# Optimization experiments

Hardware: AMD Instinct MI355X
Metric: run time of the kernel (lower is better)

The kernel has to match this reference:

```python
import jax, jax.numpy as jnp
import numpy as np

EPS = 1e-5
NEG_SLOPE = 0.2  # DGL GATConv default leaky_relu slope


def conv1d_same(x, w, b):
    # x: [N, Cin, T], w: [Cout, Cin, K]
    y = jax.lax.conv_general_dilated(x, w, (1,), 'SAME',
                                     dimension_numbers=('NCW', 'OIW', 'NCW'))
    return y + b[None, :, None]


def gated_conv(x, w1, b1, w2, b2, w3, b3):
    # Temporal_Gated_Conv: relu(conv1(x)*sigmoid(conv2(x)) + conv3(x))
    return jax.nn.relu(conv1d_same(x, w1, b1) * jax.nn.sigmoid(conv1d_same(x, w2, b2))
                       + conv1d_same(x, w3, b3))


def bn3(x, g, b):
    # BatchNorm1d on [N, C, T]: stats over (N, T), training mode (batch stats)
    m = jnp.mean(x, (0, 2), keepdims=True)
    v = jnp.var(x, (0, 2), keepdims=True)
    return (x - m) * jax.lax.rsqrt(v + EPS) * g[None, :, None] + b[None, :, None]


def bn2(x, g, b):
    # BatchNorm1d on [N, F]: stats over N
    m = jnp.mean(x, 0, keepdims=True)
    v = jnp.var(x, 0, keepdims=True)
    return (x - m) * jax.lax.rsqrt(v + EPS) * g[None, :] + b[None, :]


def setup_inputs() -> dict:
    key = jax.random.key(0)
    ks = jax.random.split(key, 24)
    N, C, T, H, DEG = 20000, 32, 8, 4, 16
    F = C * T          # GAT in/out feats per head = 256
    E = N * DEG
    s = 0.05
    inp = {
        'X': jax.random.normal(ks[0], (N, C, T), jnp.float32),
        'src': jax.random.randint(ks[1], (E,), 0, N, jnp.int32),
        'dst': jax.random.randint(ks[2], (E,), 0, N, jnp.int32),
        # residual_proj: Conv1d(C->C, k=1)
        'rp_w': jax.random.normal(ks[3], (C, C, 1), jnp.float32) * s,
        'rp_b': jnp.zeros((C,), jnp.float32),
        # gated_conv1: three Conv1d(C->C, k=3)
        'g1_w1': jax.random.normal(ks[4], (C, C, 3), jnp.float32) * s,
        'g1_b1': jnp.zeros((C,), jnp.float32),
        'g1_w2': jax.random.normal(ks[5], (C, C, 3), jnp.float32) * s,
        'g1_b2': jnp.zeros((C,), jnp.float32),
        'g1_w3': jax.random.normal(ks[6], (C, C, 3), jnp.float32) * s,
        'g1_b3': jnp.zeros((C,), jnp.float32),
        'bn0_g': jnp.ones((C,), jnp.float32),
        'bn0_b': jnp.zeros((C,), jnp.float32),
        # GATConv: fc [H*F, F], attn_l/attn_r [H, F], bias [H*F]
        'gat_w': jax.random.normal(ks[7], (H * F, F), jnp.float32) * s,
        'attn_l': jax.random.normal(ks[8], (H, F), jnp.float32) * s,
        'attn_r': jax.random.normal(ks[9], (H, F), jnp.float32) * s,
        'gat_bias': jnp.zeros((H * F,), jnp.float32),
        'bn1_g': jnp.ones((H * F,), jnp.float32),
        'bn1_b': jnp.zeros((H * F,), jnp.float32),
        # gated_conv2: three Conv1d(C*H -> C, k=3)
        'g2_w1': jax.random.normal(ks[10], (C, C * H, 3), jnp.float32) * s,
        'g2_b1': jnp.zeros((C,), jnp.float32),
        'g2_w2': jax.random.normal(ks[11], (C, C * H, 3), jnp.float32) * s,
        'g2_b2': jnp.zeros((C,), jnp.float32),
        'g2_w3': jax.random.normal(ks[12], (C, C * H, 3), jnp.float32) * s,
        'g2_b3': jnp.zeros((C,), jnp.float32),
        'bn2_g': jnp.ones((C,), jnp.float32),
        'bn2_b': jnp.zeros((C,), jnp.float32),
    }
    return inp


def reference(X, src, dst, rp_w, rp_b, g1_w1, g1_b1, g1_w2, g1_b2, g1_w3, g1_b3,
              bn0_g, bn0_b, gat_w, attn_l, attn_r, gat_bias, bn1_g, bn1_b,
              g2_w1, g2_b1, g2_w2, g2_b2, g2_w3, g2_b3, bn2_g, bn2_b):
    N, C, T = X.shape
    H, F = attn_l.shape

    residual = conv1d_same(X, rp_w, rp_b)                      # [N, C, T]
    x = gated_conv(X, g1_w1, g1_b1, g1_w2, g1_b2, g1_w3, g1_b3)
    x = bn3(x, bn0_g, bn0_b)
    x = x.reshape(N, C * T)                                    # row-major flatten == torch .view

    # --- DGL GATConv (feat_drop=attn_drop=0, concat heads, ReLU activation) ---
    h = (x @ gat_w.T).reshape(N, H, F)                         # fc projection
    el = jnp.sum(h * attn_l, -1)                               # [N, H]
    er = jnp.sum(h * attn_r, -1)                               # [N, H]
    e = jax.nn.leaky_relu(el[src] + er[dst], NEG_SLOPE)        # [E, H]
    # segment softmax over incoming edges of each dst node
    m = jax.ops.segment_max(e, dst, num_segments=N)            # [N, H]
    ee = jnp.exp(e - m[dst])
    den = jax.ops.segment_sum(ee, dst, num_segments=N)         # [N, H]
    alpha = ee / den[dst]                                      # [E, H]
    rst = jax.ops.segment_sum(alpha[:, :, None] * h[src], dst, num_segments=N)  # [N, H, F]
    rst = jax.nn.relu(rst + gat_bias.reshape(H, F))

    x = rst.reshape(N, H * F)                                  # concat heads
    x = bn2(x, bn1_g, bn1_b)
    x = x.reshape(N, (H * F) // T, T)                          # [N, C*H, T]
    x = gated_conv(x, g2_w1, g2_b1, g2_w2, g2_b2, g2_w3, g2_b3)
    x = bn3(x, bn2_g, bn2_b)
    x = jax.nn.relu(x + residual)                              # self.last=True, dropout=0
    return x
```

## Files before the change

### kernel.cpp

```cpp
#include <hip/hip_runtime.h>
#include <stdint.h>

#define NN 20000
#define NE 320000

typedef unsigned short us16;
typedef __attribute__((ext_vector_type(8))) short short8;
typedef __attribute__((ext_vector_type(4))) float f32x4;

union U4 { uint4 v; us16 s[8]; unsigned u[4]; };
union U2 { uint2 v; us16 s[4]; };

__device__ __forceinline__ float b2f(us16 u){ return __uint_as_float(((unsigned)u)<<16); }
__device__ __forceinline__ us16 f2b(float f){
  unsigned u = __float_as_uint(f);
  u += 0x7fffu + ((u>>16)&1u);
  return (us16)(u>>16);
}

__global__ __launch_bounds__(256) void k_misc(
    const float* __restrict__ gatw, us16* __restrict__ Wb,
    const float* __restrict__ w1, const float* __restrict__ w2, const float* __restrict__ w3,
    us16* __restrict__ Wt,
    const float* __restrict__ c1w1, const float* __restrict__ c1w2, const float* __restrict__ c1w3,
    const float* __restrict__ rp_w, us16* __restrict__ Wt1,
    const float* __restrict__ attnl, const float* __restrict__ attnr,
    float* __restrict__ wl, float* __restrict__ wr,
    const int* __restrict__ dst, int* __restrict__ counts)
{
  const int b = blockIdx.x, tid = threadIdx.x;
  if(b < 256){
    int i = b*256 + tid;
    float4 v = *(const float4*)(gatw + (size_t)i*4);
    U2 o;
    o.s[0]=f2b(v.x); o.s[1]=f2b(v.y); o.s[2]=f2b(v.z); o.s[3]=f2b(v.w);
    *(uint2*)(Wb + (size_t)i*4) = o.v;
  } else if(b < 400){
    int i = (b-256)*256 + tid;
    int s = i/12288, rem = i%12288;
    int co3 = rem>>7, ci = rem&127;
    const float* w = (co3<32) ? w1 : (co3<64) ? w2 : w3;
    Wt[i] = f2b(w[(co3&31)*384 + ci*3 + s]);
  } else if(b < 448){
    int i = (b-400)*256 + tid;
    int s = i>>12, rem = i&4095;
    int co3 = rem>>5, ci = rem&31;
    float v;
    if(co3 < 96){
      const float* w = (co3<32) ? c1w1 : (co3<64) ? c1w2 : c1w3;
      v = w[(co3&31)*96 + ci*3 + s];
    } else {
      v = (s==1) ? rp_w[(co3-96)*32 + ci] : 0.f;
    }
    Wt1[i] = f2b(v);
  } else if(b < 480){
    int bb = b-448;
    int sel = bb>>4, hd = (bb>>2)&3, fq = bb&3;
    const float* attn = sel ? attnr : attnl;
    int k = tid;
    float s = 0.f;
    int f0 = fq*64;
    #pragma unroll 8
    for(int f=f0; f<f0+64; f++)
      s = fmaf(attn[hd*256+f], gatw[(size_t)(hd*256+f)*256 + k], s);
    atomicAdd(&((sel ? wr : wl)[hd*256+k]), s);
  } else {
    int e = (b-480)*256 + tid;
    if(e < NE) atomicAdd(&counts[dst[e]], 1);
  }
}

__global__ __launch_bounds__(256) void k_gemm1(
    const float* __restrict__ X, const us16* __restrict__ Wt1,
    const float* __restrict__ b1, const float* __restrict__ b2, const float* __restrict__ b3,
    const float* __restrict__ rp_b,
    us16* __restrict__ gc1, us16* __restrict__ resid,
    float* __restrict__ bn0_sum, float* __restrict__ bn0_sq,
    const int* __restrict__ counts, int* __restrict__ offsets, int* __restrict__ cursor)
{
  __shared__ float smemF[5760];
  __shared__ float redS[32], redQ[32];
  __shared__ int wred[4];
  const int tid = threadIdx.x;
  if(blockIdx.x < 1250){
    us16* As = (us16*)smemF;
    us16* Bs = As + 6400;
    if(tid<32){ redS[tid]=0.f; redQ[tid]=0.f; }
    const int node0 = blockIdx.x*16;
    const int lane = tid&63, wv = tid>>6;
    const int mrow = lane&15, kg = (lane>>4)*8;
    for(int idx=tid; idx<1024; idx+=256){
      int n = idx>>6, rem = idx&63, slot = (rem>>5)*9, ci = rem&31;
      As[n*400 + slot*40 + ci] = 0;
    }
    #pragma unroll
    for(int i=0;i<4;i++){
      int idx = i*256 + tid;
      int n = idx>>6, rem = idx&63, ci = rem>>1, tq = rem&1;
      float4 xv = *(const float4*)(X + (size_t)(node0+n)*256 + ci*8 + tq*4);
      us16* p = &As[n*400 + (tq*4+1)*40 + ci];
      p[0]   = f2b(xv.x);
      p[40]  = f2b(xv.y);
      p[80]  = f2b(xv.z);
      p[120] = f2b(xv.w);
    }
    f32x4 acc[2][8] = {};
    for(int s=0; s<3; s++){
      if(s) __syncthreads();
      #pragma unroll
      for(int i=0;i<2;i++){
        int c = i*256 + tid;
        int co = c>>2, cq = c&3;
        *(uint4*)&Bs[co*40 + cq*8] = *(const uint4*)(Wt1 + s*4096 + co*32 + cq*8);
      }
      __syncthreads();
      short8 af[2], bfr[8];
      #pragma unroll
      for(int i=0;i<2;i++){
        int r = wv*32 + i*16 + mrow;
        af[i] = *(const short8*)&As[(r>>3)*400 + ((r&7)+s)*40 + kg];
      }
      #pragma unroll
      for(int j=0;j<8;j++)
        bfr[j] = *(const short8*)&Bs[(j*16 + mrow)*40 + kg];
      #pragma unroll
      for(int i=0;i<2;i++){
        #pragma unroll
        for(int j=0;j<8;j++)
          acc[i][j] = __builtin_amdgcn_mfma_f32_16x16x32_bf16(af[i], bfr[j], acc[i][j], 0, 0, 0);
      }
    }
    __syncthreads();
    us16* Og = (us16*)smemF;
    us16* Or = Og + 4096;
    const int coA = lane&15, coB = coA+16;
    const float b1A=b1[coA], b2A=b2[coA], b3A=b3[coA], brA=rp_b[coA];
    const float b1B=b1[coB], b2B=b2[coB], b3B=b3[coB], brB=rp_b[coB];
    float sA=0.f, qA=0.f, sB=0.f, qB=0.f;
    const int g = lane>>4;
    #pragma unroll
    for(int i=0;i<2;i++){
      int node = wv*4 + i*2 + (g>>1);
      int t0 = (g&1)*4;
      U2 pA, pB, rA2, rB2;
      #pragma unroll
      for(int r=0;r<4;r++){
        float c1 = acc[i][0][r]+b1A, c2 = acc[i][2][r]+b2A, c3 = acc[i][4][r]+b3A;
        float rr = acc[i][6][r]+brA;
        float sg = 1.f/(1.f+__expf(-c2));
        float v = fmaf(c1,sg,c3); v = v>0.f ? v : 0.f;
        sA += v; qA += v*v;
        pA.s[r]=f2b(v); rA2.s[r]=f2b(rr);
        c1 = acc[i][1][r]+b1B; c2 = acc[i][3][r]+b2B; c3 = acc[i][5][r]+b3B;
        rr = acc[i][7][r]+brB;
        sg = 1.f/(1.f+__expf(-c2));
        v = fmaf(c1,sg,c3); v = v>0.f ? v : 0.f;
        sB += v; qB += v*v;
        pB.s[r]=f2b(v); rB2.s[r]=f2b(rr);
      }
      *(uint2*)&Og[node*256 + coA*8 + t0] = pA.v;
      *(uint2*)&Og[node*256 + coB*8 + t0] = pB.v;
      *(uint2*)&Or[node*256 + coA*8 + t0] = rA2.v;
      *(uint2*)&Or[node*256 + coB*8 + t0] = rB2.v;
    }
    sA += __shfl_xor(sA,16,64); sA += __shfl_xor(sA,32,64);
    qA += __shfl_xor(qA,16,64); qA += __shfl_xor(qA,32,64);
    sB += __shfl_xor(sB,16,64); sB += __shfl_xor(sB,32,64);
    qB += __shfl_xor(qB,16,64); qB += __shfl_xor(qB,32,64);
    if(lane < 16){
      atomicAdd(&redS[coA], sA); atomicAdd(&redQ[coA], qA);
      atomicAdd(&redS[coB], sB); atomicAdd(&redQ[coB], qB);
    }
    __syncthreads();
    #pragma unroll
    for(int i=0;i<2;i++){
      int idx = i*256 + tid;
      *(uint4*)(gc1   + (size_t)node0*256 + (size_t)idx*8) = *(const uint4*)&Og[idx*8];
      *(uint4*)(resid + (size_t)node0*256 + (size_t)idx*8) = *(const uint4*)&Or[idx*8];
    }
    if(tid<32)      atomicAdd(&bn0_sum[tid], redS[tid]);
    else if(tid<64) atomicAdd(&bn0_sq[tid-32], redQ[tid-32]);
  } else {
    const int lane = tid&63, wv = tid>>6;
    int running = 0;
    int4 cur;
    {
      int idx = tid*4;
      cur = *(const int4*)(counts + idx);
    }
    for(int t=0; t<20; t++){
      int4 nxt; nxt.x=0; nxt.y=0; nxt.z=0; nxt.w=0;
      if(t < 19){
        int idx = (t+1)*1024 + tid*4;
        if(idx+3 < NN) nxt = *(const int4*)(counts + idx);
        else {
          if(idx   < NN) nxt.x = counts[idx];
          if(idx+1 < NN) nxt.y = counts[idx+1];
          if(idx+2 < NN) nxt.z = counts[idx+2];
          if(idx+3 < NN) nxt.w = counts[idx+3];
        }
      }
      int s = cur.x + cur.y + cur.z + cur.w;
      int incl = s;
      #pragma unroll
      for(int off=1; off<64; off<<=1){
        int v = __shfl_up(incl, off, 64);
        if(lane >= off) incl += v;
      }
      if(lane==63) wred[wv] = incl;
      __syncthreads();
      int woff = 0, btot = 0;
      #pragma unroll
      for(int w2=0; w2<4; w2++){
        int x = wred[w2];
        btot += x;
        if(w2 < wv) woff += x;
      }
      int e0 = running + woff + incl - s;
      int idx = t*1024 + tid*4;
      int4 o; o.x=e0; o.y=e0+cur.x; o.z=o.y+cur.y; o.w=o.z+cur.z;
      if(idx+3 < NN){
        *(int4*)(offsets+idx) = o;
        *(int4*)(cursor+idx)  = o;
      } else {
        if(idx   < NN){ offsets[idx]  =o.x; cursor[idx]  =o.x; }
        if(idx+1 < NN){ offsets[idx+1]=o.y; cursor[idx+1]=o.y; }
        if(idx+2 < NN){ offsets[idx+2]=o.z; cursor[idx+2]=o.z; }
        if(idx+3 < NN){ offsets[idx+3]=o.w; cursor[idx+3]=o.w; }
      }
      running += btot;
      cur = nxt;
      __syncthreads();
    }
    if(tid==0) offsets[NN] = running;
  }
}

__global__ __launch_bounds__(256) void k_eler2(const us16* __restrict__ gc1,
    const float* __restrict__ bn0_sum, const float* __restrict__ bn0_sq,
    const float* __restrict__ bn0g, const float* __restrict__ bn0b,
    const float* __restrict__ wl, const float* __restrict__ wr,
    float* __restrict__ el, float* __restrict__ er)
{
  __shared__ float sa[32], sb[32];
  const int tid = threadIdx.x;
  if(tid<32){
    float m = bn0_sum[tid]*(1.f/160000.f);
    float v = bn0_sq[tid]*(1.f/160000.f) - m*m;
    float a = bn0g[tid]*rsqrtf(v + 1e-5f);
    sa[tid] = a; sb[tid] = bn0b[tid] - m*a;
  }
  __syncthreads();
  const int wv = tid>>6, lane = tid&63;
  const int node = blockIdx.x*4 + wv;
  U2 g; g.v = *(const uint2*)(gc1 + (size_t)node*256 + lane*4);
  const float a = sa[lane>>1], b = sb[lane>>1];
  float xv[4];
  #pragma unroll
  for(int j=0;j<4;j++) xv[j] = fmaf(a, b2f(g.s[j]), b);
  float res[8];
  #pragma unroll
  for(int hd=0; hd<4; hd++){
    float4 lv = *(const float4*)(wl + hd*256 + lane*4);
    float4 rv = *(const float4*)(wr + hd*256 + lane*4);
    res[hd]   = xv[0]*lv.x + xv[1]*lv.y + xv[2]*lv.z + xv[3]*lv.w;
    res[4+hd] = xv[0]*rv.x + xv[1]*rv.y + xv[2]*rv.z + xv[3]*rv.w;
  }
  #pragma unroll
  for(int o=32;o;o>>=1){
    #pragma unroll
    for(int k=0;k<8;k++) res[k] += __shfl_xor(res[k], o, 64);
  }
  if(lane==0){
    #pragma unroll
    for(int hd=0;hd<4;hd++){ el[node*4+hd]=res[hd]; er[node*4+hd]=res[4+hd]; }
  }
}

__global__ __launch_bounds__(256) void k_scatter(const int* __restrict__ src, const int* __restrict__ dst,
    int* __restrict__ cursor, int* __restrict__ esrc,
    const float* __restrict__ el, const float* __restrict__ er,
    float* __restrict__ ew)
{
  int e = blockIdx.x*256 + threadIdx.x;
  if(e < NE){
    int s = src[e], d = dst[e];
    int pos = atomicAdd(&cursor[d], 1);
    esrc[pos] = s;
    float4 lv = *(const float4*)(el + s*4);
    float4 rv = *(const float4*)(er + d*4);
    float4 sc;
    sc.x = lv.x+rv.x; sc.x = sc.x>0.f ? sc.x : 0.2f*sc.x;
    sc.y = lv.y+rv.y; sc.y = sc.y>0.f ? sc.y : 0.2f*sc.y;
    sc.z = lv.z+rv.z; sc.z = sc.z>0.f ? sc.z : 0.2f*sc.z;
    sc.w = lv.w+rv.w; sc.w = sc.w>0.f ? sc.w : 0.2f*sc.w;
    *(float4*)(ew + (size_t)pos*4) = sc;
  }
}

__global__ __launch_bounds__(256) void k_agg2(
    const int* __restrict__ offsets, const int* __restrict__ esrc,
    const float* __restrict__ ew, const us16* __restrict__ gc1,
    const float* __restrict__ bn0_sum, const float* __restrict__ bn0_sq,
    const float* __restrict__ bn0g, const float* __restrict__ bn0b,
    us16* __restrict__ Axg)
{
  const int tid = threadIdx.x;
  const int wv = tid>>6, lane = tid&63;
  const int node = blockIdx.x*4 + wv;
  const int ch = lane>>1;
  float mmn = bn0_sum[ch]*(1.f/160000.f);
  float vvn = bn0_sq[ch]*(1.f/160000.f) - mmn*mmn;
  float sa = bn0g[ch]*rsqrtf(vvn + 1e-5f);
  float sb = bn0b[ch] - mmn*sa;
  const int beg = offsets[node];
  const int deg = offsets[node+1] - beg;
  const int h = lane>>4, i0 = lane&15;
  float m = -3.0e38f;
  for(int i=i0; i<deg; i+=16) m = fmaxf(m, ew[(size_t)(beg+i)*4 + h]);
  m = fmaxf(m, __shfl_xor(m,1,64)); m = fmaxf(m, __shfl_xor(m,2,64));
  m = fmaxf(m, __shfl_xor(m,4,64)); m = fmaxf(m, __shfl_xor(m,8,64));
  float den = 0.f;
  for(int i=i0; i<deg; i+=16) den += __expf(ew[(size_t)(beg+i)*4 + h] - m);
  den += __shfl_xor(den,1,64); den += __shfl_xor(den,2,64);
  den += __shfl_xor(den,4,64); den += __shfl_xor(den,8,64);
  const float m0=__shfl(m,0,64),   m1=__shfl(m,16,64),  m2=__shfl(m,32,64),  m3=__shfl(m,48,64);
  const float d0=__shfl(den,0,64), d1=__shfl(den,16,64),d2=__shfl(den,32,64),d3=__shfl(den,48,64);
  const float v0=d0>0.f?1.f/d0:0.f, v1=d1>0.f?1.f/d1:0.f,
              v2=d2>0.f?1.f/d2:0.f, v3=d3>0.f?1.f/d3:0.f;
  float a0c[4]={},a1c[4]={},a2c[4]={},a3c[4]={};
  #pragma unroll 4
  for(int j=0; j<deg; j++){
    int pos = beg+j;
    float4 w4 = *(const float4*)(ew + (size_t)pos*4);
    int sN = esrc[pos];
    U2 hv; hv.v = *(const uint2*)(gc1 + (size_t)sN*256 + lane*4);
    float e0 = __expf(w4.x-m0)*v0;
    float e1 = __expf(w4.y-m1)*v1;
    float e2 = __expf(w4.z-m2)*v2;
    float e3 = __expf(w4.w-m3)*v3;
    #pragma unroll
    for(int kk=0;kk<4;kk++){
      float x = b2f(hv.s[kk]);
      a0c[kk] = fmaf(e0,x,a0c[kk]);
      a1c[kk] = fmaf(e1,x,a1c[kk]);
      a2c[kk] = fmaf(e2,x,a2c[kk]);
      a3c[kk] = fmaf(e3,x,a3c[kk]);
    }
  }
  const float sbi = sb * ((deg>0)?1.f:0.f);
  U2 o0,o1,o2,o3;
  #pragma unroll
  for(int kk=0;kk<4;kk++){
    o0.s[kk]=f2b(fmaf(sa,a0c[kk],sbi));
    o1.s[kk]=f2b(fmaf(sa,a1c[kk],sbi));
    o2.s[kk]=f2b(fmaf(sa,a2c[kk],sbi));
    o3.s[kk]=f2b(fmaf(sa,a3c[kk],sbi));
  }
  *(uint2*)(Axg + ((size_t)node)*256            + lane*4) = o0.v;
  *(uint2*)(Axg + ((size_t)NN + node)*256       + lane*4) = o1.v;
  *(uint2*)(Axg + ((size_t)2*NN + node)*256     + lane*4) = o2.v;
  *(uint2*)(Axg + ((size_t)3*NN + node)*256     + lane*4) = o3.v;
}

__global__ __launch_bounds__(256) void k_gemm3(const us16* __restrict__ Axg, const us16* __restrict__ Wb,
    const float* __restrict__ gbias, us16* __restrict__ rst,
    float* __restrict__ bn1_sum, float* __restrict__ bn1_sq)
{
  const int tid = threadIdx.x;
  const int row0 = blockIdx.x*128;
  const int cb   = blockIdx.y*128;
  const int hd   = blockIdx.z;
  const us16* A = Axg + (size_t)hd*NN*256;
  const us16* B = Wb  + (size_t)(hd*256 + cb)*256;
  const int lane = tid&63, wv = tid>>6;
  const int wm = wv&1, wn = wv>>1;
  const int mrow = lane&15, kg = (lane>>4)*8;
  const short8 zz = {0,0,0,0,0,0,0,0};
  int ga[4];
  #pragma unroll
  for(int i=0;i<4;i++) ga[i] = row0 + wm*64 + i*16 + mrow;
  f32x4 acc[4][4] = {};
  #pragma unroll 2
  for(int k0=0; k0<256; k0+=32){
    short8 af[4], bfr[4];
    #pragma unroll
    for(int i=0;i<4;i++)
      af[i] = (ga[i] < NN) ? *(const short8*)(A + (size_t)ga[i]*256 + k0 + kg) : zz;
    #pragma unroll
    for(int j=0;j<4;j++)
      bfr[j] = *(const short8*)(B + (size_t)(wn*64 + j*16 + mrow)*256 + k0 + kg);
    #pragma unroll
    for(int i=0;i<4;i++){
      #pragma unroll
      for(int j=0;j<4;j++)
        acc[i][j] = __builtin_amdgcn_mfma_f32_16x16x32_bf16(af[i], bfr[j], acc[i][j], 0, 0, 0);
    }
  }
  float gb[4];
  #pragma unroll
  for(int j=0;j<4;j++)
    gb[j] = gbias[hd*256 + cb + wn*64 + j*16 + (lane&15)];
  float cs[4]={}, cq[4]={};
  #pragma unroll
  for(int i=0;i<4;i++){
    #pragma unroll
    for(int j=0;j<4;j++){
      #pragma unroll
      for(int r=0;r<4;r++){
        int g = row0 + wm*64 + i*16 + (lane>>4)*4 + r;
        if(g < NN){
          float v = acc[i][j][r] + gb[j];
          v = v>0.f ? v : 0.f;
          rst[(size_t)g*1024 + hd*256 + cb + wn*64 + j*16 + (lane&15)] = f2b(v);
          cs[j] += v; cq[j] += v*v;
        }
      }
    }
  }
  #pragma unroll
  for(int j=0;j<4;j++){
    cs[j] += __shfl_xor(cs[j],16,64); cs[j] += __shfl_xor(cs[j],32,64);
    cq[j] += __shfl_xor(cq[j],16,64); cq[j] += __shfl_xor(cq[j],32,64);
  }
  if(lane < 16){
    #pragma unroll
    for(int j=0;j<4;j++){
      int col = hd*256 + cb + wn*64 + j*16 + lane;
      atomicAdd(&bn1_sum[col], cs[j]);
      atomicAdd(&bn1_sq[col],  cq[j]);
    }
  }
}

__global__ __launch_bounds__(256) void k_gemm2(
    const us16* __restrict__ rst, const us16* __restrict__ Wt,
    const float* __restrict__ bn1_sum, const float* __restrict__ bn1_sq,
    const float* __restrict__ bn1g, const float* __restrict__ bn1b,
    const float* __restrict__ b1, const float* __restrict__ b2, const float* __restrict__ b3,
    us16* __restrict__ y2, float* __restrict__ bn2_sum, float* __restrict__ bn2_sq)
{
  __shared__ float smemF[7808];
  float* s1a = smemF;
  float* s1b = smemF + 1024;
  us16* As = (us16*)(smemF + 2048);
  __shared__ float redS[32], redQ[32];
  const int tid = threadIdx.x;
  if(tid<32){ redS[tid]=0.f; redQ[tid]=0.f; }
  const int node0 = blockIdx.x*16;
  const int lane = tid&63, wv = tid>>6;
  const int mrow = lane&15, kg = (lane>>4)*8;
  for(int f=tid; f<1024; f+=256){
    float m = bn1_sum[f]*(1.f/20000.f);
    float v = bn1_sq[f]*(1.f/20000.f) - m*m;
    float a = bn1g[f]*rsqrtf(v + 1e-5f);
    int l = (f&7)*128 + (f>>3);
    s1a[l] = a; s1b[l] = bn1b[f] - m*a;
  }
  for(int idx=tid; idx<2048; idx+=256){
    int n = idx>>7, rem = idx&127, slot = (rem>>6)*9, ci = rem&63;
    As[n*720 + slot*72 + ci] = 0;
  }
  __syncthreads();
  f32x4 acc[2][6] = {};
  for(int kc=0; kc<2; kc++){
    if(kc) __syncthreads();
    #pragma unroll
    for(int i=0;i<4;i++){
      int idx = i*256 + tid;
      int n = idx>>6, cil = idx&63;
      int ci = kc*64 + cil;
      U4 in; in.v = *(const uint4*)(rst + (size_t)(node0+n)*1024 + ci*8);
      us16* p = &As[n*720 + 72 + cil];
      #pragma unroll
      for(int t=0;t<8;t++){
        float a = s1a[t*128+ci], b = s1b[t*128+ci];
        p[t*72] = f2b(fmaf(a, b2f(in.s[t]), b));
      }
    }
    __syncthreads();
    #pragma unroll
    for(int s=0; s<3; s++){
      #pragma unroll
      for(int kk=0; kk<64; kk+=32){
        short8 af[2], bfr[6];
        #pragma unroll
        for(int i=0;i<2;i++){
          int r = wv*32 + i*16 + mrow;
          af[i] = *(const short8*)&As[(r>>3)*720 + ((r&7)+s)*72 + kk + kg];
        }
        #pragma unroll
        for(int j=0;j<6;j++)
          bfr[j] = *(const short8*)(Wt + s*12288 + (j*16 + mrow)*128 + kc*64 + kk + kg);
        #pragma unroll
        for(int i=0;i<2;i++){
          #pragma unroll
          for(int j=0;j<6;j++)
            acc[i][j] = __builtin_amdgcn_mfma_f32_16x16x32_bf16(af[i], bfr[j], acc[i][j], 0, 0, 0);
        }
      }
    }
  }
  __syncthreads();
  us16* Og = (us16*)smemF;
  const int coA = lane&15, coB = coA+16;
  const float b1A=b1[coA], b2A=b2[coA], b3A=b3[coA];
  const float b1B=b1[coB], b2B=b2[coB], b3B=b3[coB];
  float sA=0.f, qA=0.f, sB=0.f, qB=0.f;
  const int g = lane>>4;
  #pragma unroll
  for(int i=0;i<2;i++){
    int node = wv*4 + i*2 + (g>>1);
    int t0 = (g&1)*4;
    U2 pA, pB;
    #pragma unroll
    for(int r=0;r<4;r++){
      float c1 = acc[i][0][r]+b1A, c2 = acc[i][2][r]+b2A, c3 = acc[i][4][r]+b3A;
      float sg = 1.f/(1.f+__expf(-c2));
      float v = fmaf(c1,sg,c3); v = v>0.f ? v : 0.f;
      sA += v; qA += v*v; pA.s[r]=f2b(v);
      c1 = acc[i][1][r]+b1B; c2 = acc[i][3][r]+b2B; c3 = acc[i][5][r]+b3B;
      sg = 1.f/(1.f+__expf(-c2));
      v = fmaf(c1,sg,c3); v = v>0.f ? v : 0.f;
      sB += v; qB += v*v; pB.s[r]=f2b(v);
    }
    *(uint2*)&Og[node*256 + coA*8 + t0] = pA.v;
    *(uint2*)&Og[node*256 + coB*8 + t0] = pB.v;
  }
  sA += __shfl_xor(sA,16,64); sA += __shfl_xor(sA,32,64);
  qA += __shfl_xor(qA,16,64); qA += __shfl_xor(qA,32,64);
  sB += __shfl_xor(sB,16,64); sB += __shfl_xor(sB,32,64);
  qB += __shfl_xor(qB,16,64); qB += __shfl_xor(qB,32,64);
  if(lane < 16){
    atomicAdd(&redS[coA], sA); atomicAdd(&redQ[coA], qA);
    atomicAdd(&redS[coB], sB); atomicAdd(&redQ[coB], qB);
  }
  __syncthreads();
  #pragma unroll
  for(int i=0;i<2;i++){
    int idx = i*256 + tid;
    *(uint4*)(y2 + (size_t)node0*256 + (size_t)idx*8) = *(const uint4*)&Og[idx*8];
  }
  if(tid<32)      atomicAdd(&bn2_sum[tid], redS[tid]);
  else if(tid<64) atomicAdd(&bn2_sq[tid-32], redQ[tid-32]);
}

__global__ __launch_bounds__(256) void k_final(const us16* __restrict__ y2,
    const float* __restrict__ bn2_sum, const float* __restrict__ bn2_sq,
    const float* __restrict__ bn2g, const float* __restrict__ bn2b,
    const us16* __restrict__ resid, float* __restrict__ out)
{
  __shared__ float fa[32], fb[32];
  const int tid = threadIdx.x;
  if(tid<32){
    float m = bn2_sum[tid]*(1.f/160000.f);
    float v = bn2_sq[tid]*(1.f/160000.f) - m*m;
    float a = bn2g[tid]*rsqrtf(v + 1e-5f);
    fa[tid] = a; fb[tid] = bn2b[tid] - m*a;
  }
  __syncthreads();
  size_t base = ((size_t)blockIdx.x*256 + tid)*8;
  int ch = (int)((base>>3)&31);
  float a = fa[ch], b = fb[ch];
  U4 yv, rv;
  yv.v = *(const uint4*)(y2+base);
  rv.v = *(const uint4*)(resid+base);
  float4 o0, o1;
  float vv[8];
  #pragma unroll
  for(int j=0;j<8;j++){
    float v = fmaf(a, b2f(yv.s[j]), b) + b2f(rv.s[j]);
    vv[j] = v>0.f ? v : 0.f;
  }
  o0.x=vv[0]; o0.y=vv[1]; o0.z=vv[2]; o0.w=vv[3];
  o1.x=vv[4]; o1.y=vv[5]; o1.z=vv[6]; o1.w=vv[7];
  *(float4*)(out+base)   = o0;
  *(float4*)(out+base+4) = o1;
}

extern "C" void kernel_launch(void* const* d_in, const int* in_sizes, int n_in,
                              void* d_out, int out_size, void* d_ws, size_t ws_size,
                              hipStream_t stream)
{
  const float* X    = (const float*)d_in[0];
  const int*  src   = (const int*)d_in[1];
  const int*  dst   = (const int*)d_in[2];
  const float* rp_w = (const float*)d_in[3];
  const float* rp_b = (const float*)d_in[4];
  const float* g1w1 = (const float*)d_in[5];
  const float* g1b1 = (const float*)d_in[6];
  const float* g1w2 = (const float*)d_in[7];
  const float* g1b2 = (const float*)d_in[8];
  const float* g1w3 = (const float*)d_in[9];
  const float* g1b3 = (const float*)d_in[10];
  const float* bn0g = (const float*)d_in[11];
  const float* bn0b = (const float*)d_in[12];
  const float* gatw = (const float*)d_in[13];
  const float* attnl= (const float*)d_in[14];
  const float* attnr= (const float*)d_in[15];
  const float* gbias= (const float*)d_in[16];
  const float* bn1g = (const float*)d_in[17];
  const float* bn1b = (const float*)d_in[18];
  const float* g2w1 = (const float*)d_in[19];
  const float* g2b1 = (const float*)d_in[20];
  const float* g2w2 = (const float*)d_in[21];
  const float* g2b2 = (const float*)d_in[22];
  const float* g2w3 = (const float*)d_in[23];
  const float* g2b3 = (const float*)d_in[24];
  const float* bn2g = (const float*)d_in[25];
  const float* bn2b = (const float*)d_in[26];
  float* out = (float*)d_out;
  (void)in_sizes; (void)n_in; (void)out_size; (void)ws_size;

  char* w = (char*)d_ws;
  float* bn0_sum = (float*)w;
  float* bn0_sq  = bn0_sum + 32;
  float* bn1_sum = bn0_sum + 64;
  float* bn1_sq  = bn1_sum + 1024;
  float* bn2_sum = bn1_sq  + 1024;
  float* bn2_sq  = bn2_sum + 32;
  float* wl      = bn2_sq + 32;
  float* wr      = wl + 1024;
  int*   counts  = (int*)(wr + 1024);
  size_t zeroBytes = (size_t)((char*)(counts + NN) - w);
  int*   offsets = counts + NN;
  int*   cursor  = offsets + 20004;
  int*   esrc    = cursor + NN;
  float* el      = (float*)(esrc + NE);
  float* er      = el + NN*4;
  float* ew      = er + NN*4;
  us16*  wb      = (us16*)(ew + (size_t)NE*4);
  us16*  resid   = wb + 262144;
  us16*  gc1     = resid + 5120000;
  us16*  Axg     = gc1   + 5120000;
  us16*  rst     = Axg   + 20480000;
  us16*  Wt      = rst   + 20480000;
  us16*  Wt1     = Wt    + 36864;
  us16*  y2      = gc1;

  hipMemsetAsync(d_ws, 0, zeroBytes, stream);
  k_misc<<<1730, 256, 0, stream>>>(gatw, wb, g2w1, g2w2, g2w3, Wt,
                                   g1w1, g1w2, g1w3, rp_w, Wt1,
                                   attnl, attnr, wl, wr, dst, counts);
  k_gemm1<<<1251, 256, 0, stream>>>(X, Wt1, g1b1, g1b2, g1b3, rp_b,
                                    gc1, resid, bn0_sum, bn0_sq,
                                    counts, offsets, cursor);
  k_eler2<<<5000, 256, 0, stream>>>(gc1, bn0_sum, bn0_sq, bn0g, bn0b, wl, wr, el, er);
  k_scatter<<<1250, 256, 0, stream>>>(src, dst, cursor, esrc, el, er, ew);
  k_agg2<<<5000, 256, 0, stream>>>(offsets, esrc, ew, gc1, bn0_sum, bn0_sq, bn0g, bn0b, Axg);
  k_gemm3<<<dim3(157, 2, 4), 256, 0, stream>>>(Axg, wb, gbias, rst, bn1_sum, bn1_sq);
  k_gemm2<<<1250, 256, 0, stream>>>(rst, Wt, bn1_sum, bn1_sq, bn1g, bn1b,
                                    g2b1, g2b2, g2b3, y2, bn2_sum, bn2_sq);
  k_final<<<2500, 256, 0, stream>>>(y2, bn2_sum, bn2_sq, bn2g, bn2b, resid, out);
}
```

Before: 396.8 us.

## Stage GEMM operands through LDS with direct global-to-LDS loads and swizzle

Result: faster. 348.1 us (-12.3%).

```diff
diff --git a/kernel.cpp b/kernel.cpp
--- a/kernel.cpp
+++ b/kernel.cpp
@@ -16,6 +16,11 @@
   unsigned u = __float_as_uint(f);
   u += 0x7fffu + ((u>>16)&1u);
   return (us16)(u>>16);
+}
+
+__device__ __forceinline__ void gll16(const void* g, void* l){
+  __builtin_amdgcn_global_load_lds((const __attribute__((address_space(1))) void*)g,
+                                   (__attribute__((address_space(3))) void*)l, 16, 0, 0);
 }
 
 __global__ __launch_bounds__(256) void k_misc(
@@ -367,6 +372,8 @@
     const float* __restrict__ gbias, us16* __restrict__ rst,
     float* __restrict__ bn1_sum, float* __restrict__ bn1_sq)
 {
+  __shared__ us16 As[4096];
+  __shared__ us16 Bs[4096];
   const int tid = threadIdx.x;
   const int row0 = blockIdx.x*128;
   const int cb   = blockIdx.y*128;
@@ -375,21 +382,39 @@
   const us16* B = Wb  + (size_t)(hd*256 + cb)*256;
   const int lane = tid&63, wv = tid>>6;
   const int wm = wv&1, wn = wv>>1;
-  const int mrow = lane&15, kg = (lane>>4)*8;
-  const short8 zz = {0,0,0,0,0,0,0,0};
-  int ga[4];
-  #pragma unroll
-  for(int i=0;i<4;i++) ga[i] = row0 + wm*64 + i*16 + mrow;
+  const int mrow = lane&15, g4 = lane>>4;
+  const us16* sgA[2]; const us16* sgB[2];
+  us16* sdA[2]; us16* sdB[2];
+  #pragma unroll
+  for(int i=0;i<2;i++){
+    int r = (i*4+wv)*16 + (lane>>2);
+    int c = (lane&3) ^ (r&3);
+    int ga = row0 + r; if(ga >= NN) ga = NN-1;
+    sgA[i] = A + (size_t)ga*256 + c*8;
+    sgB[i] = B + (size_t)r*256 + c*8;
+    sdA[i] = As + (i*4+wv)*512;
+    sdB[i] = Bs + (i*4+wv)*512;
+  }
   f32x4 acc[4][4] = {};
-  #pragma unroll 2
   for(int k0=0; k0<256; k0+=32){
+    if(k0) __syncthreads();
+    #pragma unroll
+    for(int i=0;i<2;i++){
+      gll16(sgA[i] + k0, sdA[i]);
+      gll16(sgB[i] + k0, sdB[i]);
+    }
+    __syncthreads();
     short8 af[4], bfr[4];
     #pragma unroll
-    for(int i=0;i<4;i++)
-      af[i] = (ga[i] < NN) ? *(const short8*)(A + (size_t)ga[i]*256 + k0 + kg) : zz;
-    #pragma unroll
-    for(int j=0;j<4;j++)
-      bfr[j] = *(const short8*)(B + (size_t)(wn*64 + j*16 + mrow)*256 + k0 + kg);
+    for(int i=0;i<4;i++){
+      int r = wm*64 + i*16 + mrow;
+      af[i] = *(const short8*)&As[r*32 + ((g4 ^ (r&3))<<3)];
+    }
+    #pragma unroll
+    for(int j=0;j<4;j++){
+      int r = wn*64 + j*16 + mrow;
+      bfr[j] = *(const short8*)&Bs[r*32 + ((g4 ^ (r&3))<<3)];
+    }
     #pragma unroll
     for(int i=0;i<4;i++){
       #pragma unroll
@@ -440,30 +465,41 @@
     const float* __restrict__ b1, const float* __restrict__ b2, const float* __restrict__ b3,
     us16* __restrict__ y2, float* __restrict__ bn2_sum, float* __restrict__ bn2_sq)
 {
-  __shared__ float smemF[7808];
-  float* s1a = smemF;
-  float* s1b = smemF + 1024;
-  us16* As = (us16*)(smemF + 2048);
+  __shared__ us16 As[11520];
+  __shared__ us16 Bs[6912];
   __shared__ float redS[32], redQ[32];
   const int tid = threadIdx.x;
   if(tid<32){ redS[tid]=0.f; redQ[tid]=0.f; }
   const int node0 = blockIdx.x*16;
   const int lane = tid&63, wv = tid>>6;
   const int mrow = lane&15, kg = (lane>>4)*8;
-  for(int f=tid; f<1024; f+=256){
-    float m = bn1_sum[f]*(1.f/20000.f);
-    float v = bn1_sq[f]*(1.f/20000.f) - m*m;
-    float a = bn1g[f]*rsqrtf(v + 1e-5f);
-    int l = (f&7)*128 + (f>>3);
-    s1a[l] = a; s1b[l] = bn1b[f] - m*a;
-  }
   for(int idx=tid; idx<2048; idx+=256){
     int n = idx>>7, rem = idx&127, slot = (rem>>6)*9, ci = rem&63;
     As[n*720 + slot*72 + ci] = 0;
   }
-  __syncthreads();
   f32x4 acc[2][6] = {};
   for(int kc=0; kc<2; kc++){
+    float ra[8], rb[8];
+    {
+      int f0 = (kc*64 + (tid&63))*8;
+      float4 s0 = *(const float4*)(bn1_sum + f0), s1 = *(const float4*)(bn1_sum + f0 + 4);
+      float4 q0 = *(const float4*)(bn1_sq  + f0), q1 = *(const float4*)(bn1_sq  + f0 + 4);
+      float4 g0 = *(const float4*)(bn1g    + f0), g1 = *(const float4*)(bn1g    + f0 + 4);
+      float4 h0 = *(const float4*)(bn1b    + f0), h1 = *(const float4*)(bn1b    + f0 + 4);
+      const float* sp = (const float*)&s0; const float* qp = (const float*)&q0;
+      const float* gp = (const float*)&g0; const float* hp = (const float*)&h0;
+      #pragma unroll
+      for(int t=0;t<8;t++){
+        float sv = (t<4)? sp[t] : ((const float*)&s1)[t-4];
+        float qv = (t<4)? qp[t] : ((const float*)&q1)[t-4];
+        float gv = (t<4)? gp[t] : ((const float*)&g1)[t-4];
+        float hv = (t<4)? hp[t] : ((const float*)&h1)[t-4];
+        float m = sv*(1.f/20000.f);
+        float v = qv*(1.f/20000.f) - m*m;
+        float a = gv*rsqrtf(v + 1e-5f);
+        ra[t] = a; rb[t] = hv - m*a;
+      }
+    }
     if(kc) __syncthreads();
     #pragma unroll
     for(int i=0;i<4;i++){
@@ -473,14 +509,19 @@
       U4 in; in.v = *(const uint4*)(rst + (size_t)(node0+n)*1024 + ci*8);
       us16* p = &As[n*720 + 72 + cil];
       #pragma unroll
-      for(int t=0;t<8;t++){
-        float a = s1a[t*128+ci], b = s1b[t*128+ci];
-        p[t*72] = f2b(fmaf(a, b2f(in.s[t]), b));
-      }
-    }
-    __syncthreads();
-    #pragma unroll
+      for(int t=0;t<8;t++)
+        p[t*72] = f2b(fmaf(ra[t], b2f(in.s[t]), rb[t]));
+    }
     for(int s=0; s<3; s++){
+      if(s) __syncthreads();
+      #pragma unroll
+      for(int i=0;i<3;i++){
+        int chunk = i*256 + tid;
+        int brow = chunk>>3, cc = chunk&7;
+        *(uint4*)&Bs[brow*72 + cc*8] =
+          *(const uint4*)(Wt + s*12288 + brow*128 + kc*64 + cc*8);
+      }
+      __syncthreads();
       #pragma unroll
       for(int kk=0; kk<64; kk+=32){
         short8 af[2], bfr[6];
@@ -491,7 +532,7 @@
         }
         #pragma unroll
         for(int j=0;j<6;j++)
-          bfr[j] = *(const short8*)(Wt + s*12288 + (j*16 + mrow)*128 + kc*64 + kk + kg);
+          bfr[j] = *(const short8*)&Bs[(j*16 + mrow)*72 + kk + kg];
         #pragma unroll
         for(int i=0;i<2;i++){
           #pragma unroll
@@ -502,7 +543,7 @@
     }
   }
   __syncthreads();
-  us16* Og = (us16*)smemF;
+  us16* Og = (us16*)As;
   const int coA = lane&15, coB = coA+16;
   const float b1A=b1[coA], b2A=b2[coA], b3A=b3[coA];
   const float b1B=b1[coB], b2B=b2[coB], b3B=b3[coB];
```
